# Kernel tuning notes

Measured on AMD Instinct MI355X. Metric: run time of the kernel, lower is better.

## Reference

```python
import jax, jax.numpy as jnp
import numpy as np

B = 8192          # batch rows
F0 = 2048         # base input features
E = 512           # embed rows added per recursion level
L = 3             # chain depth
OUT = 2048        # MAIN output dim
NNZ_E = 8192      # nnz per embed sparse weight (~16/row)
NNZ_M = 16384     # nnz of MAIN sparse weight (~8/row)


def _spmm_t(rows, cols, vals, x, n_rows):
    """Compute (W_sparse @ x.T).T = x @ W.T for COO W of shape [n_rows, x.shape[1]].
    out[b, r] = sum_{k: rows[k]==r} vals[k] * x[b, cols[k]]
    """
    contrib = x[:, cols] * vals                     # [B, nnz]
    return jax.ops.segment_sum(contrib.T, rows, num_segments=n_rows).T  # [B, n_rows]


def setup_inputs() -> dict:
    key = jax.random.key(0)
    ks = jax.random.split(key, 12)
    widths = [F0, F0 + E, F0 + 2 * E]               # input width at each recursion level
    inp = {"x": jax.random.normal(ks[0], (B, F0), dtype=jnp.float32)}
    for i, w in enumerate(widths):
        inp[f"emb_rows{i}"] = jax.random.randint(ks[1 + 3 * i], (NNZ_E,), 0, E, dtype=jnp.int32)
        inp[f"emb_cols{i}"] = jax.random.randint(ks[2 + 3 * i], (NNZ_E,), 0, w, dtype=jnp.int32)
        inp[f"emb_vals{i}"] = jax.random.normal(ks[3 + 3 * i], (NNZ_E,), dtype=jnp.float32)
    inp["main_rows"] = jax.random.randint(ks[10], (NNZ_M,), 0, OUT, dtype=jnp.int32)
    inp["main_cols"] = jax.random.randint(ks[11], (NNZ_M,), 0, F0 + 3 * E, dtype=jnp.int32)
    inp["main_vals"] = jax.random.normal(jax.random.fold_in(key, 99), (NNZ_M,), dtype=jnp.float32)
    return inp


def reference(x, emb_rows0, emb_cols0, emb_vals0,
              emb_rows1, emb_cols1, emb_vals1,
              emb_rows2, emb_cols2, emb_vals2,
              main_rows, main_cols, main_vals):
    # Recursive chain unrolled oldest-first: each level sparse-mms its embed
    # weight against the running input and concatenates the result.
    h = x
    for rows, cols, vals in ((emb_rows0, emb_cols0, emb_vals0),
                             (emb_rows1, emb_cols1, emb_vals1),
                             (emb_rows2, emb_cols2, emb_vals2)):
        e = _spmm_t(rows, cols, vals, h, E)         # [B, E]
        h = jnp.concatenate([h, e], axis=1)
    # is_last: pass concatenated features through the MAIN sparse linear
    return _spmm_t(main_rows, main_cols, main_vals, h, OUT)  # [B, OUT]
```

## Files before the change

### kernel.cpp

```cpp
#include <hip/hip_runtime.h>
#include <stdint.h>

#define F0    2048
#define EROWS 512
#define NOUT  2048
#define MROWS 8192

typedef __attribute__((ext_vector_type(8))) short bf16x8;
typedef __attribute__((ext_vector_type(4))) float f32x4;
typedef __attribute__((ext_vector_type(8))) unsigned short u16x8;

typedef const __attribute__((address_space(1))) unsigned char ga_t;
typedef __attribute__((address_space(3))) unsigned char lds_t;

__device__ __forceinline__ void async_load16(const void* g, void* l) {
  __builtin_amdgcn_global_load_lds((ga_t*)g, (lds_t*)l, 16, 0, 0);
}

__device__ __forceinline__ unsigned short f2bf(float f) {
  unsigned int u = __builtin_bit_cast(unsigned int, f);
  u += 0x7fffu + ((u >> 16) & 1u);
  return (unsigned short)(u >> 16);
}

__global__ __launch_bounds__(256) void csr_cast_kernel(
    const int* __restrict__ r0, const int* __restrict__ c0, const float* __restrict__ v0, int n0,
    const int* __restrict__ r1, const int* __restrict__ c1, const float* __restrict__ v1, int n1,
    const int* __restrict__ r2, const int* __restrict__ c2, const float* __restrict__ v2, int n2,
    const int* __restrict__ rm, const int* __restrict__ cm, const float* __restrict__ vm, int nm,
    int* __restrict__ rp_all, int* __restrict__ cc_all, float* __restrict__ cv_all)
{
  const int b = blockIdx.x;
  const int tid = threadIdx.x;

  const int* rows; const int* cols; const float* vals; int nnz, nrows;
  if      (b == 0) { rows = r0; cols = c0; vals = v0; nnz = n0; nrows = EROWS; }
  else if (b == 1) { rows = r1; cols = c1; vals = v1; nnz = n1; nrows = EROWS; }
  else if (b == 2) { rows = r2; cols = c2; vals = v2; nnz = n2; nrows = EROWS; }
  else             { rows = rm; cols = cm; vals = vm; nnz = nm; nrows = NOUT; }
  int* rp  = rp_all + b * 4096;
  int* cc  = cc_all + b * 8192;
  float* cv = cv_all + b * 8192;

  __shared__ int hist[NOUT + 1];
  __shared__ int tsum[256];

  for (int i = tid; i < nrows; i += 256) hist[i] = 0;
  __syncthreads();

  int k0 = 0;
  for (; k0 + 2048 <= nnz; k0 += 2048) {
    const int kk = k0 + tid * 8;
    int4 ra = *(const int4*)(rows + kk);
    int4 rb = *(const int4*)(rows + kk + 4);
    atomicAdd(&hist[ra.x], 1); atomicAdd(&hist[ra.y], 1);
    atomicAdd(&hist[ra.z], 1); atomicAdd(&hist[ra.w], 1);
    atomicAdd(&hist[rb.x], 1); atomicAdd(&hist[rb.y], 1);
    atomicAdd(&hist[rb.z], 1); atomicAdd(&hist[rb.w], 1);
  }
  for (int k = k0 + tid; k < nnz; k += 256) atomicAdd(&hist[rows[k]], 1);
  __syncthreads();

  const int per = nrows >> 8;
  const int base = tid * per;
  int sum = 0;
  for (int i = 0; i < per; ++i) sum += hist[base + i];
  tsum[tid] = sum;
  __syncthreads();
  for (int off = 1; off < 256; off <<= 1) {
    int add = (tid >= off) ? tsum[tid - off] : 0;
    __syncthreads();
    tsum[tid] += add;
    __syncthreads();
  }
  int run = (tid == 0) ? 0 : tsum[tid - 1];
  for (int i = 0; i < per; ++i) { int h = hist[base + i]; hist[base + i] = run; run += h; }
  __syncthreads();

  for (int i = tid; i < nrows; i += 256) rp[i] = hist[i];
  if (tid == 0) rp[nrows] = nnz;
  __syncthreads();

  k0 = 0;
  for (; k0 + 2048 <= nnz; k0 += 2048) {
    const int kk = k0 + tid * 8;
    int4   ra = *(const int4*)(rows + kk);
    int4   rb = *(const int4*)(rows + kk + 4);
    int4   ca = *(const int4*)(cols + kk);
    int4   cb2 = *(const int4*)(cols + kk + 4);
    float4 va = *(const float4*)(vals + kk);
    float4 vb = *(const float4*)(vals + kk + 4);
    int p;
    p = atomicAdd(&hist[ra.x], 1); cc[p] = ca.x;  cv[p] = va.x;
    p = atomicAdd(&hist[ra.y], 1); cc[p] = ca.y;  cv[p] = va.y;
    p = atomicAdd(&hist[ra.z], 1); cc[p] = ca.z;  cv[p] = va.z;
    p = atomicAdd(&hist[ra.w], 1); cc[p] = ca.w;  cv[p] = va.w;
    p = atomicAdd(&hist[rb.x], 1); cc[p] = cb2.x; cv[p] = vb.x;
    p = atomicAdd(&hist[rb.y], 1); cc[p] = cb2.y; cv[p] = vb.y;
    p = atomicAdd(&hist[rb.z], 1); cc[p] = cb2.z; cv[p] = vb.z;
    p = atomicAdd(&hist[rb.w], 1); cc[p] = cb2.w; cv[p] = vb.w;
  }
  for (int k = k0 + tid; k < nnz; k += 256) {
    int p = atomicAdd(&hist[rows[k]], 1);
    cc[p] = cols[k]; cv[p] = vals[k];
  }
}

template <bool BF16OUT>
__global__ __launch_bounds__(256) void expand_csr_kernel(
    const int* __restrict__ rp, const int* __restrict__ cc,
    const float* __restrict__ cv, const float* __restrict__ Dsrc,
    void* __restrict__ out, int nrows,
    const float* __restrict__ x, unsigned short* __restrict__ Ab, int cast_base)
{
  const int b = blockIdx.x;
  const int tid = threadIdx.x;

  if (b >= nrows) {
    const int cb = cast_base + (b - nrows);
    const float4* xp = (const float4*)x;
    u16x8* ap = (u16x8*)Ab;
#pragma unroll
    for (int it = 0; it < 4; ++it) {
      int i = cb * 1024 + it * 256 + tid;
      float4 a = xp[2 * i], c = xp[2 * i + 1];
      u16x8 o;
      o[0] = f2bf(a.x); o[1] = f2bf(a.y); o[2] = f2bf(a.z); o[3] = f2bf(a.w);
      o[4] = f2bf(c.x); o[5] = f2bf(c.y); o[6] = f2bf(c.z); o[7] = f2bf(c.w);
      ap[i] = o;
    }
    return;
  }

  const int r = b;
  __shared__ float acc[F0];
  __shared__ int   icol[128];
  __shared__ float ival[128];
  __shared__ int   icnt;

  float4* a4 = (float4*)acc;
  a4[tid * 2]     = (float4){0.f, 0.f, 0.f, 0.f};
  a4[tid * 2 + 1] = (float4){0.f, 0.f, 0.f, 0.f};
  if (tid == 0) icnt = 0;
  __syncthreads();

  const int s = rp[r], e = rp[r + 1];
  for (int i = s + tid; i < e; i += 256) {
    int c = cc[i]; float v = cv[i];
    if (c < F0) atomicAdd(&acc[c], v);
    else { int p = atomicAdd(&icnt, 1); if (p < 128) { icol[p] = c - F0; ival[p] = v; } }
  }
  __syncthreads();
  int n = icnt; if (n > 128) n = 128;

  float4 q0 = a4[tid * 2], q1 = a4[tid * 2 + 1];
  for (int j = 0; j < n; ++j) {
    const float4* src = (const float4*)(Dsrc + (size_t)icol[j] * F0) + tid * 2;
    float v = ival[j];
    float4 s0 = src[0], s1 = src[1];
    q0.x += v * s0.x; q0.y += v * s0.y; q0.z += v * s0.z; q0.w += v * s0.w;
    q1.x += v * s1.x; q1.y += v * s1.y; q1.z += v * s1.z; q1.w += v * s1.w;
  }

  if (BF16OUT) {
    u16x8 o;
    o[0] = f2bf(q0.x); o[1] = f2bf(q0.y); o[2] = f2bf(q0.z); o[3] = f2bf(q0.w);
    o[4] = f2bf(q1.x); o[5] = f2bf(q1.y); o[6] = f2bf(q1.z); o[7] = f2bf(q1.w);
    ((u16x8*)out)[(size_t)r * 256 + tid] = o;
  } else {
    float4* dst = (float4*)out + (size_t)r * 512 + tid * 2;
    dst[0] = q0; dst[1] = q1;
  }
}

__global__ __launch_bounds__(512, 2) void gemm256_kernel(
    const unsigned short* __restrict__ A, const unsigned short* __restrict__ B,
    float* __restrict__ C)
{
  constexpr int K  = F0;
  constexpr int N  = NOUT;
  constexpr int NT = K / 64;

  extern __shared__ __align__(16) unsigned short lds[];
  unsigned short* sA = lds;
  unsigned short* sB = lds + 32768;

  const int tid  = threadIdx.x;
  const int lane = tid & 63;
  const int w    = tid >> 6;
  const int wr   = w >> 2;
  const int wc   = w & 3;
  const int mm   = lane & 15;
  const int g    = lane >> 4;
  const int sx   = mm & 7;

  const int flat = blockIdx.y * 8 + blockIdx.x;
  const int nid  = (flat & 7) * 32 + (flat >> 3);
  const int bm   = nid >> 3;
  const int bn   = nid & 7;

  const unsigned short* Ag = A + (size_t)bm * 256 * K;
  const unsigned short* Bg = B + (size_t)bn * 256 * K;

  const int    r0    = tid >> 3;
  const int    c0    = (tid & 7) ^ (r0 & 7);
  const size_t gA0   = (size_t)((r0 & 63) + (r0 >> 6) * 128) * K + c0 * 8;
  const size_t gB0   = (size_t)((r0 & 31) + (r0 >> 5) * 64)  * K + c0 * 8;
  const int    loff0 = tid * 8;
  const int    loff1 = 4096 + tid * 8;

#define STG_A(buf, qm, t) do {                                                \
    async_load16(Ag + gA0 + (size_t)(qm) * 64 * K + (size_t)(t) * 64,         \
                 sA + (buf) * 16384 + (qm) * 8192 + loff0);                   \
    async_load16(Ag + gA0 + (size_t)(qm) * 64 * K + (size_t)128 * K +         \
                 (size_t)(t) * 64,                                            \
                 sA + (buf) * 16384 + (qm) * 8192 + loff1);                   \
  } while (0)

#define STG_B(buf, qn, t) do {                                                \
    async_load16(Bg + gB0 + (size_t)(qn) * 32 * K + (size_t)(t) * 64,         \
                 sB + (buf) * 16384 + (qn) * 8192 + loff0);                   \
    async_load16(Bg + gB0 + (size_t)(qn) * 32 * K + (size_t)128 * K +         \
                 (size_t)(t) * 64,                                            \
                 sB + (buf) * 16384 + (qn) * 8192 + loff1);                   \
  } while (0)

  const unsigned short* paB = sA + (wr * 64 + mm) * 64;
  const unsigned short* pbB = sB + (wc * 32 + mm) * 64;
  const int s0 = ((0 * 4 + g) ^ sx) * 8;
  const int s1 = ((1 * 4 + g) ^ sx) * 8;

  bf16x8 afP[4][2];
  bf16x8 afQ[4][2];
  bf16x8 bf0A[2][2], bf0B[2][2];
  bf16x8 bf1[2][2];

#define LDA(dst, buf, qm) do {                                                \
    const unsigned short* p_ = paB + (buf) * 16384 + (qm) * 8192;             \
    _Pragma("unroll") for (int tm = 0; tm < 4; ++tm) {                        \
      dst[tm][0] = *(const bf16x8*)(p_ + tm * 1024 + s0);                     \
      dst[tm][1] = *(const bf16x8*)(p_ + tm * 1024 + s1);                     \
    } } while (0)

#define LDB(dst, buf, qn) do {                                                \
    const unsigned short* p_ = pbB + (buf) * 16384 + (qn) * 8192;             \
    _Pragma("unroll") for (int tn = 0; tn < 2; ++tn) {                        \
      dst[tn][0] = *(const bf16x8*)(p_ + tn * 1024 + s0);                     \
      dst[tn][1] = *(const bf16x8*)(p_ + tn * 1024 + s1);                     \
    } } while (0)

#define MFMA_Q(qm, qn, afX, bfX) do {                                         \
    __builtin_amdgcn_s_setprio(1);                                            \
    _Pragma("unroll") for (int tm = 0; tm < 4; ++tm)                          \
    _Pragma("unroll") for (int tn = 0; tn < 2; ++tn) {                        \
      acc[(qm)*4+tm][(qn)*2+tn] = __builtin_amdgcn_mfma_f32_16x16x32_bf16(    \
          afX[tm][0], bfX[tn][0], acc[(qm)*4+tm][(qn)*2+tn], 0, 0, 0);        \
      acc[(qm)*4+tm][(qn)*2+tn] = __builtin_amdgcn_mfma_f32_16x16x32_bf16(    \
          afX[tm][1], bfX[tn][1], acc[(qm)*4+tm][(qn)*2+tn], 0, 0, 0);        \
    }                                                                         \
    __builtin_amdgcn_s_setprio(0);                                            \
  } while (0)

#define CFENCE     asm volatile("" ::: "memory")
#define BAR        do { CFENCE; __builtin_amdgcn_s_barrier(); CFENCE; } while (0)
#define SCHED0     __builtin_amdgcn_sched_barrier(0)
#define WAIT_VM(n) asm volatile("s_waitcnt vmcnt(" #n ")" ::: "memory")

  f32x4 acc[8][4];
#pragma unroll
  for (int i = 0; i < 8; ++i)
#pragma unroll
    for (int j = 0; j < 4; ++j) acc[i][j] = (f32x4)0.f;

  STG_B(0, 0, 0); STG_B(0, 1, 0);
  STG_A(0, 0, 0); STG_A(0, 1, 0);
  STG_B(1, 0, 1); STG_B(1, 1, 1);
  STG_A(1, 0, 1);
  WAIT_VM(6);
  BAR; SCHED0;
  LDA(afP, 0, 0);
  LDB(bf0A, 0, 0);

#define TILE(buf, nbuf, BF0C, BF0N, t) do {                                   \
                                                                      \
    STG_A(nbuf, 1, (t) + 1);                                     \
    LDB(bf1, buf, 1);                           \
    MFMA_Q(0, 0, afP, BF0C);                                                  \
                                                                      \
    WAIT_VM(8);                                             \
    BAR; SCHED0;                                                              \
    LDA(afQ, buf, 1);                                                         \
    MFMA_Q(0, 1, afP, bf1);                                                   \
                                                                      \
    STG_B(buf, 0, (t) + 2);                     \
    WAIT_VM(2);                                   \
    BAR; SCHED0;                                                              \
    LDA(afP, nbuf, 0);                                          \
    MFMA_Q(1, 1, afQ, bf1);                                                   \
                                                         \
    STG_B(buf, 1, (t) + 2);                             \
    STG_A(buf, 0, (t) + 2);                             \
    LDB(BF0N, nbuf, 0);                           \
    MFMA_Q(1, 0, afQ, BF0C);                                                  \
  } while (0)

  for (int tp = 0; tp < 15; ++tp) {
    const int t0 = 2 * tp;
    TILE(0, 1, bf0A, bf0B, t0);
    TILE(1, 0, bf0B, bf0A, t0 + 1);
  }

  {
    STG_A(1, 1, 31);
    LDB(bf1, 0, 1);
    MFMA_Q(0, 0, afP, bf0A);
    WAIT_VM(8); BAR; SCHED0;
    LDA(afQ, 0, 1);
    MFMA_Q(0, 1, afP, bf1);
    WAIT_VM(2); BAR; SCHED0;
    LDA(afP, 1, 0);
    MFMA_Q(1, 1, afQ, bf1);
    LDB(bf0B, 1, 0);
    MFMA_Q(1, 0, afQ, bf0A);
  }
  {
    LDB(bf1, 1, 1);
    MFMA_Q(0, 0, afP, bf0B);
    WAIT_VM(0); BAR; SCHED0;
    LDA(afQ, 1, 1);
    MFMA_Q(0, 1, afP, bf1);
    MFMA_Q(1, 1, afQ, bf1);
    MFMA_Q(1, 0, afQ, bf0B);
  }

  const int rowb = bm * 256 + wr * 128 + g * 4;
  const int colb = bn * 256 + wc * 64 + mm;
#pragma unroll
  for (int im = 0; im < 8; ++im) {
#pragma unroll
    for (int in2 = 0; in2 < 4; ++in2) {
      const int row = rowb + im * 16;
      const int col = colb + in2 * 16;
#pragma unroll
      for (int r = 0; r < 4; ++r)
        C[(size_t)(row + r) * N + col] = acc[im][in2][r];
    }
  }

#undef STG_A
#undef STG_B
#undef LDA
#undef LDB
#undef MFMA_Q
#undef TILE
#undef CFENCE
#undef BAR
#undef SCHED0
#undef WAIT_VM
}

extern "C" void kernel_launch(void* const* d_in, const int* in_sizes, int n_in,
                              void* d_out, int out_size, void* d_ws, size_t ws_size,
                              hipStream_t stream)
{
  const float* x   = (const float*)d_in[0];
  const int*   er0 = (const int*)d_in[1];
  const int*   ec0 = (const int*)d_in[2];
  const float* ev0 = (const float*)d_in[3];
  const int*   er1 = (const int*)d_in[4];
  const int*   ec1 = (const int*)d_in[5];
  const float* ev1 = (const float*)d_in[6];
  const int*   er2 = (const int*)d_in[7];
  const int*   ec2 = (const int*)d_in[8];
  const float* ev2 = (const float*)d_in[9];
  const int*   mr  = (const int*)d_in[10];
  const int*   mc  = (const int*)d_in[11];
  const float* mv  = (const float*)d_in[12];
  const int nnz_e0 = in_sizes[1];
  const int nnz_e1 = in_sizes[4];
  const int nnz_e2 = in_sizes[7];
  const int nnz_m  = in_sizes[10];

  int*   rp_all = (int*)d_ws;
  int*   cc_all = rp_all + 4 * 4096;
  float* cv_all = (float*)(cc_all + 48 * 1024);
  float* D      = (float*)(cv_all + 48 * 1024);
  unsigned short* Mb = (unsigned short*)(D + (size_t)3 * EROWS * F0);
  unsigned short* Ab = Mb + (size_t)NOUT * F0;

  hipLaunchKernelGGL(csr_cast_kernel, dim3(4), dim3(256), 0, stream,
                     er0, ec0, ev0, nnz_e0,
                     er1, ec1, ev1, nnz_e1,
                     er2, ec2, ev2, nnz_e2,
                     mr,  mc,  mv,  nnz_m,
                     rp_all, cc_all, cv_all);

  hipLaunchKernelGGL((expand_csr_kernel<false>), dim3(EROWS + 512), dim3(256), 0, stream,
                     rp_all + 0 * 4096, cc_all + 0 * 8192, cv_all + 0 * 8192,
                     D, (void*)D, EROWS, x, Ab, 0);
  hipLaunchKernelGGL((expand_csr_kernel<false>), dim3(EROWS + 512), dim3(256), 0, stream,
                     rp_all + 1 * 4096, cc_all + 1 * 8192, cv_all + 1 * 8192,
                     D, (void*)(D + (size_t)EROWS * F0), EROWS, x, Ab, 512);
  hipLaunchKernelGGL((expand_csr_kernel<false>), dim3(EROWS + 512), dim3(256), 0, stream,
                     rp_all + 2 * 4096, cc_all + 2 * 8192, cv_all + 2 * 8192,
                     D, (void*)(D + (size_t)2 * EROWS * F0), EROWS, x, Ab, 1024);
  hipLaunchKernelGGL((expand_csr_kernel<true>), dim3(NOUT + 512), dim3(256), 0, stream,
                     rp_all + 3 * 4096, cc_all + 3 * 8192, cv_all + 3 * 8192,
                     D, (void*)Mb, NOUT, x, Ab, 1536);

  hipFuncSetAttribute(reinterpret_cast<const void*>(gemm256_kernel),
                      hipFuncAttributeMaxDynamicSharedMemorySize, 131072);
  hipLaunchKernelGGL(gemm256_kernel, dim3(NOUT / 256, MROWS / 256), dim3(512),
                     131072, stream, Ab, Mb, (float*)d_out);
}
```

Baseline: 227.2 us.

## Replace COO-to-CSR conversion with per-row full scan of COO entries

Removes the single-kernel COO-to-CSR bucketing pass, which ran on only four blocks. Each expand block now scans the whole COO row array with int4 loads and keeps the entries matching its own row. This saves one serialized launch and a low-parallelism prologue. In exchange, every block reads all nnz row indices (8K or 16K ints), so total L2 traffic grows by a factor of nrows.

```diff
diff --git a/kernel.cpp b/kernel.cpp
--- a/kernel.cpp
+++ b/kernel.cpp
@@ -23,94 +23,11 @@
   return (unsigned short)(u >> 16);
 }
 
-__global__ __launch_bounds__(256) void csr_cast_kernel(
-    const int* __restrict__ r0, const int* __restrict__ c0, const float* __restrict__ v0, int n0,
-    const int* __restrict__ r1, const int* __restrict__ c1, const float* __restrict__ v1, int n1,
-    const int* __restrict__ r2, const int* __restrict__ c2, const float* __restrict__ v2, int n2,
-    const int* __restrict__ rm, const int* __restrict__ cm, const float* __restrict__ vm, int nm,
-    int* __restrict__ rp_all, int* __restrict__ cc_all, float* __restrict__ cv_all)
-{
-  const int b = blockIdx.x;
-  const int tid = threadIdx.x;
-
-  const int* rows; const int* cols; const float* vals; int nnz, nrows;
-  if      (b == 0) { rows = r0; cols = c0; vals = v0; nnz = n0; nrows = EROWS; }
-  else if (b == 1) { rows = r1; cols = c1; vals = v1; nnz = n1; nrows = EROWS; }
-  else if (b == 2) { rows = r2; cols = c2; vals = v2; nnz = n2; nrows = EROWS; }
-  else             { rows = rm; cols = cm; vals = vm; nnz = nm; nrows = NOUT; }
-  int* rp  = rp_all + b * 4096;
-  int* cc  = cc_all + b * 8192;
-  float* cv = cv_all + b * 8192;
-
-  __shared__ int hist[NOUT + 1];
-  __shared__ int tsum[256];
-
-  for (int i = tid; i < nrows; i += 256) hist[i] = 0;
-  __syncthreads();
-
-  int k0 = 0;
-  for (; k0 + 2048 <= nnz; k0 += 2048) {
-    const int kk = k0 + tid * 8;
-    int4 ra = *(const int4*)(rows + kk);
-    int4 rb = *(const int4*)(rows + kk + 4);
-    atomicAdd(&hist[ra.x], 1); atomicAdd(&hist[ra.y], 1);
-    atomicAdd(&hist[ra.z], 1); atomicAdd(&hist[ra.w], 1);
-    atomicAdd(&hist[rb.x], 1); atomicAdd(&hist[rb.y], 1);
-    atomicAdd(&hist[rb.z], 1); atomicAdd(&hist[rb.w], 1);
-  }
-  for (int k = k0 + tid; k < nnz; k += 256) atomicAdd(&hist[rows[k]], 1);
-  __syncthreads();
-
-  const int per = nrows >> 8;
-  const int base = tid * per;
-  int sum = 0;
-  for (int i = 0; i < per; ++i) sum += hist[base + i];
-  tsum[tid] = sum;
-  __syncthreads();
-  for (int off = 1; off < 256; off <<= 1) {
-    int add = (tid >= off) ? tsum[tid - off] : 0;
-    __syncthreads();
-    tsum[tid] += add;
-    __syncthreads();
-  }
-  int run = (tid == 0) ? 0 : tsum[tid - 1];
-  for (int i = 0; i < per; ++i) { int h = hist[base + i]; hist[base + i] = run; run += h; }
-  __syncthreads();
-
-  for (int i = tid; i < nrows; i += 256) rp[i] = hist[i];
-  if (tid == 0) rp[nrows] = nnz;
-  __syncthreads();
-
-  k0 = 0;
-  for (; k0 + 2048 <= nnz; k0 += 2048) {
-    const int kk = k0 + tid * 8;
-    int4   ra = *(const int4*)(rows + kk);
-    int4   rb = *(const int4*)(rows + kk + 4);
-    int4   ca = *(const int4*)(cols + kk);
-    int4   cb2 = *(const int4*)(cols + kk + 4);
-    float4 va = *(const float4*)(vals + kk);
-    float4 vb = *(const float4*)(vals + kk + 4);
-    int p;
-    p = atomicAdd(&hist[ra.x], 1); cc[p] = ca.x;  cv[p] = va.x;
-    p = atomicAdd(&hist[ra.y], 1); cc[p] = ca.y;  cv[p] = va.y;
-    p = atomicAdd(&hist[ra.z], 1); cc[p] = ca.z;  cv[p] = va.z;
-    p = atomicAdd(&hist[ra.w], 1); cc[p] = ca.w;  cv[p] = va.w;
-    p = atomicAdd(&hist[rb.x], 1); cc[p] = cb2.x; cv[p] = vb.x;
-    p = atomicAdd(&hist[rb.y], 1); cc[p] = cb2.y; cv[p] = vb.y;
-    p = atomicAdd(&hist[rb.z], 1); cc[p] = cb2.z; cv[p] = vb.z;
-    p = atomicAdd(&hist[rb.w], 1); cc[p] = cb2.w; cv[p] = vb.w;
-  }
-  for (int k = k0 + tid; k < nnz; k += 256) {
-    int p = atomicAdd(&hist[rows[k]], 1);
-    cc[p] = cols[k]; cv[p] = vals[k];
-  }
-}
-
 template <bool BF16OUT>
-__global__ __launch_bounds__(256) void expand_csr_kernel(
-    const int* __restrict__ rp, const int* __restrict__ cc,
-    const float* __restrict__ cv, const float* __restrict__ Dsrc,
-    void* __restrict__ out, int nrows,
+__global__ __launch_bounds__(256) void expand_scan_kernel(
+    const int* __restrict__ rows, const int* __restrict__ cols,
+    const float* __restrict__ vals, int nnz,
+    const float* __restrict__ Dsrc, void* __restrict__ out, int nrows,
     const float* __restrict__ x, unsigned short* __restrict__ Ab, int cast_base)
 {
   const int b = blockIdx.x;
@@ -144,12 +61,25 @@
   if (tid == 0) icnt = 0;
   __syncthreads();
 
-  const int s = rp[r], e = rp[r + 1];
-  for (int i = s + tid; i < e; i += 256) {
-    int c = cc[i]; float v = cv[i];
-    if (c < F0) atomicAdd(&acc[c], v);
-    else { int p = atomicAdd(&icnt, 1); if (p < 128) { icol[p] = c - F0; ival[p] = v; } }
-  }
+#define HANDLE(kk) do {                                                       \
+    int c_ = cols[kk]; float v_ = vals[kk];                                   \
+    if (c_ < F0) atomicAdd(&acc[c_], v_);                                     \
+    else { int p_ = atomicAdd(&icnt, 1);                                      \
+           if (p_ < 128) { icol[p_] = c_ - F0; ival[p_] = v_; } }             \
+  } while (0)
+
+  const int n4 = nnz >> 2;
+  for (int gq = tid; gq < n4; gq += 256) {
+    const int k = gq * 4;
+    int4 rr = *(const int4*)(rows + k);
+    if (rr.x == r) HANDLE(k);
+    if (rr.y == r) HANDLE(k + 1);
+    if (rr.z == r) HANDLE(k + 2);
+    if (rr.w == r) HANDLE(k + 3);
+  }
+  for (int k = (n4 << 2) + tid; k < nnz; k += 256)
+    if (rows[k] == r) HANDLE(k);
+#undef HANDLE
   __syncthreads();
   int n = icnt; if (n > 128) n = 128;
 
@@ -283,24 +213,24 @@
 
 #define TILE(buf, nbuf, BF0C, BF0N, t) do {                                   \
                                                                       \
-    STG_A(nbuf, 1, (t) + 1);                                     \
-    LDB(bf1, buf, 1);                           \
+    STG_A(nbuf, 1, (t) + 1);                                                  \
+    LDB(bf1, buf, 1);                                                         \
     MFMA_Q(0, 0, afP, BF0C);                                                  \
                                                                       \
-    WAIT_VM(8);                                             \
+    WAIT_VM(8);                                                               \
     BAR; SCHED0;                                                              \
     LDA(afQ, buf, 1);                                                         \
     MFMA_Q(0, 1, afP, bf1);                                                   \
                                                                       \
-    STG_B(buf, 0, (t) + 2);                     \
-    WAIT_VM(2);                                   \
+    STG_B(buf, 0, (t) + 2);                                                   \
+    WAIT_VM(2);                                                               \
     BAR; SCHED0;                                                              \
-    LDA(afP, nbuf, 0);                                          \
+    LDA(afP, nbuf, 0);                                                        \
     MFMA_Q(1, 1, afQ, bf1);                                                   \
-                                                         \
-    STG_B(buf, 1, (t) + 2);                             \
-    STG_A(buf, 0, (t) + 2);                             \
-    LDB(BF0N, nbuf, 0);                           \
+                                                                      \
+    STG_B(buf, 1, (t) + 2);                                                   \
+    STG_A(buf, 0, (t) + 2);                                                   \
+    LDB(BF0N, nbuf, 0);                                                       \
     MFMA_Q(1, 0, afQ, BF0C);                                                  \
   } while (0)
 
@@ -388,24 +318,17 @@
   unsigned short* Mb = (unsigned short*)(D + (size_t)3 * EROWS * F0);
   unsigned short* Ab = Mb + (size_t)NOUT * F0;
 
-  hipLaunchKernelGGL(csr_cast_kernel, dim3(4), dim3(256), 0, stream,
+  hipLaunchKernelGGL((expand_scan_kernel<false>), dim3(EROWS + 512), dim3(256), 0, stream,
                      er0, ec0, ev0, nnz_e0,
+                     D, (void*)D, EROWS, x, Ab, 0);
+  hipLaunchKernelGGL((expand_scan_kernel<false>), dim3(EROWS + 512), dim3(256), 0, stream,
                      er1, ec1, ev1, nnz_e1,
+                     D, (void*)(D + (size_t)EROWS * F0), EROWS, x, Ab, 512);
+  hipLaunchKernelGGL((expand_scan_kernel<false>), dim3(EROWS + 512), dim3(256), 0, stream,
                      er2, ec2, ev2, nnz_e2,
-                     mr,  mc,  mv,  nnz_m,
-                     rp_all, cc_all, cv_all);
-
-  hipLaunchKernelGGL((expand_csr_kernel<false>), dim3(EROWS + 512), dim3(256), 0, stream,
-                     rp_all + 0 * 4096, cc_all + 0 * 8192, cv_all + 0 * 8192,
-                     D, (void*)D, EROWS, x, Ab, 0);
-  hipLaunchKernelGGL((expand_csr_kernel<false>), dim3(EROWS + 512), dim3(256), 0, stream,
-                     rp_all + 1 * 4096, cc_all + 1 * 8192, cv_all + 1 * 8192,
-                     D, (void*)(D + (size_t)EROWS * F0), EROWS, x, Ab, 512);
-  hipLaunchKernelGGL((expand_csr_kernel<false>), dim3(EROWS + 512), dim3(256), 0, stream,
-                     rp_all + 2 * 4096, cc_all + 2 * 8192, cv_all + 2 * 8192,
                      D, (void*)(D + (size_t)2 * EROWS * F0), EROWS, x, Ab, 1024);
-  hipLaunchKernelGGL((expand_csr_kernel<true>), dim3(NOUT + 512), dim3(256), 0, stream,
-                     rp_all + 3 * 4096, cc_all + 3 * 8192, cv_all + 3 * 8192,
+  hipLaunchKernelGGL((expand_scan_kernel<true>), dim3(NOUT + 512), dim3(256), 0, stream,
+                     mr, mc, mv, nnz_m,
                      D, (void*)Mb, NOUT, x, Ab, 1536);
 
   hipFuncSetAttribute(reinterpret_cast<const void*>(gemm256_kernel),
```

Result: faster. 220.2 us (-3.0%).
